# Kernel optimization log

Measured on AMD Instinct MI355X. Metric: run time of the kernel, lower is better.

The kernel has to match this reference:

```python
import jax, jax.numpy as jnp
import numpy as np

NUM_HEADS = 4
INITIAL_VALUE = 1.0
HEADS_RANGE = 3.0


def rotate_every_two(x):
    x1 = x[..., ::2]
    x2 = x[..., 1::2]
    return jnp.stack([-x2, x1], axis=-1).reshape(x.shape)


def theta_shift(x, sin, cos):
    return x * cos + rotate_every_two(x) * sin


def rel_pos_2d(h, w, key_dim):
    # angle: repeat each frequency twice -> length key_dim
    base = 1.0 / 10000.0 ** jnp.linspace(0.0, 1.0, key_dim // 2)
    angle = jnp.repeat(base, 2)
    decay = jnp.log(1.0 - 2.0 ** (-(INITIAL_VALUE + HEADS_RANGE * jnp.arange(NUM_HEADS, dtype=jnp.float32) / NUM_HEADS)))
    idx = jnp.arange(h * w, dtype=jnp.float32)
    sin = jnp.sin(idx[:, None] * angle[None, :]).reshape(h, w, key_dim)
    cos = jnp.cos(idx[:, None] * angle[None, :]).reshape(h, w, key_dim)
    def decay_1d(l):
        i = jnp.arange(l, dtype=jnp.float32)
        return jnp.abs(i[:, None] - i[None, :])[None, :, :] * decay[:, None, None]  # (n, l, l)
    return sin, cos, decay_1d(h), decay_1d(w)


def setup_inputs() -> dict:
    key = jax.random.key(0)
    b, C, H, W = 16, 256, 64, 64
    ks = jax.random.split(key, 12)
    gain = 2.0 ** (-2.5)
    xav = (2.0 / (C + C)) ** 0.5
    return {
        "x": jax.random.normal(ks[0], (b, C, H, W), jnp.float32),
        "Wq": jax.random.normal(ks[1], (C, C), jnp.float32) * gain * xav,
        "bq": jnp.zeros((C,), jnp.float32),
        "Wk": jax.random.normal(ks[2], (C, C), jnp.float32) * gain * xav,
        "bk": jnp.zeros((C,), jnp.float32),
        "Wv": jax.random.normal(ks[3], (C, C), jnp.float32) * gain * xav,
        "bv": jnp.zeros((C,), jnp.float32),
        "dw_kernel": jax.random.normal(ks[4], (5, 5, 1, C), jnp.float32) * 0.05,
        "dw_bias": jnp.zeros((C,), jnp.float32),
        "Wo": jax.random.normal(ks[5], (C, C), jnp.float32) * xav,
        "bo": jnp.zeros((C,), jnp.float32),
    }


def reference(x, Wq, bq, Wk, bk, Wv, bv, dw_kernel, dw_bias, Wo, bo):
    x = jnp.transpose(x, (0, 2, 3, 1))  # (b, h, w, c)
    b, h, w, c = x.shape
    n = NUM_HEADS
    d = c // n  # key_dim == head_dim (value_factor=1)
    scaling = d ** (-0.5)

    sin, cos, mask_h, mask_w = rel_pos_2d(h, w, d)

    q = x @ Wq + bq
    k = (x @ Wk + bk) * scaling
    v = x @ Wv + bv  # (b, h, w, c)

    # depthwise 5x5 conv (lepe) on v, NHWC
    lepe = jax.lax.conv_general_dilated(
        v, dw_kernel, window_strides=(1, 1), padding=((2, 2), (2, 2)),
        dimension_numbers=("NHWC", "HWIO", "NHWC"), feature_group_count=c,
    ) + dw_bias

    q = q.reshape(b, h, w, n, d).transpose(0, 3, 1, 2, 4)  # (b, n, h, w, d)
    k = k.reshape(b, h, w, n, d).transpose(0, 3, 1, 2, 4)
    qr = theta_shift(q, sin, cos)  # sin/cos (h,w,d) broadcast
    kr = theta_shift(k, sin, cos)

    # width-axis attention: rows independent
    qr_w = qr.transpose(0, 2, 1, 3, 4)  # (b, h, n, w, d)
    kr_w = kr.transpose(0, 2, 1, 3, 4)
    v5 = v.reshape(b, h, w, n, d).transpose(0, 1, 3, 2, 4)  # (b, h, n, w, d)
    qk_w = jnp.einsum("bhnqd,bhnkd->bhnqk", qr_w, kr_w) + mask_w  # (b,h,n,w,w)
    v5 = jnp.einsum("bhnqk,bhnkd->bhnqd", jax.nn.softmax(qk_w, axis=-1), v5)

    # height-axis attention: columns independent
    qr_h = qr.transpose(0, 3, 1, 2, 4)  # (b, w, n, h, d)
    kr_h = kr.transpose(0, 3, 1, 2, 4)
    v6 = v5.transpose(0, 3, 2, 1, 4)  # (b, w, n, h, d)
    qk_h = jnp.einsum("bwnqd,bwnkd->bwnqk", qr_h, kr_h) + mask_h  # (b,w,n,h,h)
    out = jnp.einsum("bwnqk,bwnkd->bwnqd", jax.nn.softmax(qk_h, axis=-1), v6)

    out = out.transpose(0, 3, 1, 2, 4).reshape(b, h, w, c)  # (b,h,w,n*d)
    out = (out + lepe) @ Wo + bo
    return jnp.transpose(out, (0, 3, 1, 2))  # (b, c, h, w)
```

## Files before the change

### kernel.cpp

```cpp
#include <hip/hip_runtime.h>
#include <hip/hip_bf16.h>

typedef unsigned short u16;
typedef unsigned int   u32;
typedef __attribute__((ext_vector_type(8))) short bf16x8;
typedef __attribute__((ext_vector_type(4))) float f32x4;

__device__ __forceinline__ float bf2f(u16 u) {
    union { u32 i; float f; } x; x.i = ((u32)u) << 16; return x.f;
}
__device__ __forceinline__ u16 f2bf(float f) {
    union { float f; u32 i; } x; x.f = f;
    u32 i = x.i;
    u32 r = (i + 0x7fffu + ((i >> 16) & 1u)) >> 16;
    return (u16)r;
}

__device__ __forceinline__ void gload16(const void* g, void* l) {
    __builtin_amdgcn_global_load_lds(
        (const __attribute__((address_space(1))) void*)g,
        (__attribute__((address_space(3))) void*)l, 16, 0, 0);
}

__global__ void k_tables(float2* __restrict__ csT) {
    int id = blockIdx.x * 256 + threadIdx.x;
    int t = id >> 5, i = id & 31;
    double ang = pow(10000.0, -(double)i / 31.0);
    double a = (double)t * ang;
    csT[id] = make_float2((float)cos(a), (float)sin(a));
}

__global__ __launch_bounds__(256) void k_prep_w(
    const float* __restrict__ Wq, const float* __restrict__ Wk,
    const float* __restrict__ Wv, const float* __restrict__ Wo,
    u16* __restrict__ WTq, u16* __restrict__ WTk,
    u16* __restrict__ WTv, u16* __restrict__ WoT)
{
    __shared__ float T[32][33];
    int z = blockIdx.z;
    const float* W = (z == 0) ? Wq : (z == 1) ? Wk : (z == 2) ? Wv : Wo;
    u16* WT        = (z == 0) ? WTq : (z == 1) ? WTk : (z == 2) ? WTv : WoT;
    int n0 = blockIdx.x * 32, k0 = blockIdx.y * 32;
    int tx = threadIdx.x & 31, ty = threadIdx.x >> 5;
#pragma unroll
    for (int i = 0; i < 4; i++)
        T[ty * 4 + i][tx] = W[(k0 + ty * 4 + i) * 256 + n0 + tx];
    __syncthreads();
#pragma unroll
    for (int i = 0; i < 4; i++)
        WT[(n0 + ty * 4 + i) * 256 + k0 + tx] = f2bf(T[tx][ty * 4 + i]);
}

__global__ __launch_bounds__(512, 1) void k_qkv_fused(
    const float* __restrict__ x, const u16* __restrict__ WTall,
    const float* __restrict__ bq, const float* __restrict__ bk,
    const float* __restrict__ bv,
    const float2* __restrict__ csT,
    u16* __restrict__ qr, u16* __restrict__ kr, u16* __restrict__ vO,
    u16* __restrict__ v5)
{
    __shared__ alignas(16) char smem[163840];
    u16* Alds = (u16*)smem;
    u16* BldsA[2] = { (u16*)(smem + 65536),
                      (u16*)(smem + 98304) };
    float2* SL = (float2*)(smem + 131072);

    const int tid = threadIdx.x;
    const int t0 = blockIdx.x * 128;
    const int lane = tid & 63, w = tid >> 6;

    const int srcChunk = (lane & 7) ^ (lane >> 3);
    const int rowInGrp = lane >> 3;

    {
        float* Bf = (float*)(smem + 65536);
        const int b0 = t0 >> 12, sb0 = t0 & 4095;
        const float* xb = x + ((size_t)b0 * 256) * 4096 + sb0;
#pragma unroll
        for (int ch = 0; ch < 2; ++ch) {
#pragma unroll
            for (int p = 0; p < 8; ++p) {
                int it = p * 512 + tid;
                int c = it >> 5, s4 = (it & 31) * 4;
                float4 v4 = *(const float4*)(xb + (size_t)(ch * 128 + c) * 4096 + s4);
                *(float4*)(Bf + c * 128 + s4) = v4;
            }
            __syncthreads();
#pragma unroll
            for (int p = 0; p < 4; ++p) {
                int it = p * 512 + tid;
                int tok = it & 127, ck = it >> 7;
                u16 tmp[8];
#pragma unroll
                for (int j = 0; j < 8; ++j)
                    tmp[j] = f2bf(Bf[(ck * 8 + j) * 128 + tok]);
                int gc = ch * 16 + ck;
                int gcs = (gc & 24) | ((gc & 7) ^ (tok & 7));
                *(bf16x8*)(Alds + tok * 256 + gcs * 8) = *(bf16x8*)tmp;
            }
            __syncthreads();
        }
    }

#pragma unroll
    for (int q = 0; q < 4; ++q) {
        int rl = (w * 4 + q) * 8 + rowInGrp;
        gload16(WTall + (size_t)rl * 256 + srcChunk * 8,
                BldsA[0] + (size_t)(w * 4 + q) * 512);
    }

    {
        const int sb = t0 & 4095;
#pragma unroll
        for (int p = 0; p < 8; ++p) {
            int idx = p * 512 + tid;
            SL[idx] = csT[(size_t)sb * 32 + idx];
        }
    }
    __syncthreads();

    const int wr = w >> 2, wc = w & 3;
    const int l15 = lane & 15, l4 = lane >> 4, l7 = lane & 7;

    f32x4 acc[4][4];

#pragma unroll
    for (int mat = 0; mat < 3; ++mat) {
#pragma unroll
        for (int mi = 0; mi < 4; ++mi)
#pragma unroll
            for (int ni = 0; ni < 4; ++ni) acc[mi][ni] = (f32x4)0.f;

#pragma unroll
        for (int ks = 0; ks < 4; ++ks) {
            const int s = mat * 4 + ks;
            u16* Bl = BldsA[s & 1];
            if (s < 11) {
                const int s2 = s + 1;
                const int mat2 = s2 >> 2, ks2 = s2 & 3;
#pragma unroll
                for (int q = 0; q < 4; ++q) {
                    int rl = (w * 4 + q) * 8 + rowInGrp;
                    gload16(WTall + (size_t)mat2 * 65536 + (size_t)rl * 256 +
                                ks2 * 64 + srcChunk * 8,
                            BldsA[s2 & 1] + (size_t)(w * 4 + q) * 512);
                }
            }
#pragma unroll
            for (int kk = 0; kk < 2; ++kk) {
                bf16x8 af[4], bfr[4];
#pragma unroll
                for (int mi = 0; mi < 4; ++mi) {
                    int r = wr * 64 + mi * 16 + l15;
                    af[mi] = *(const bf16x8*)(Alds + r * 256 + (ks * 8 + ((kk * 4 + l4) ^ l7)) * 8);
                }
#pragma unroll
                for (int ni = 0; ni < 4; ++ni) {
                    int r = wc * 64 + ni * 16 + l15;
                    bfr[ni] = *(const bf16x8*)(Bl + r * 64 + ((kk * 4 + l4) ^ l7) * 8);
                }
#pragma unroll
                for (int mi = 0; mi < 4; ++mi)
#pragma unroll
                    for (int ni = 0; ni < 4; ++ni)
                        acc[mi][ni] = __builtin_amdgcn_mfma_f32_16x16x32_bf16(
                            af[mi], bfr[ni], acc[mi][ni], 0, 0, 0);
            }
            __syncthreads();
        }

        const float* bias = (mat == 0) ? bq : (mat == 1) ? bk : bv;
        u16* out          = (mat == 0) ? qr : (mat == 1) ? kr : vO;
        const float kscale = (mat == 1) ? 0.125f : 1.0f;
        float bcol[4]; int ip[4];
#pragma unroll
        for (int ni = 0; ni < 4; ++ni) {
            bcol[ni] = bias[wc * 64 + ni * 16 + l15];
            ip[ni] = (ni * 16 + l15) >> 1;
        }
#pragma unroll
        for (int mi = 0; mi < 4; ++mi) {
#pragma unroll
            for (int rg = 0; rg < 4; ++rg) {
                const int sl = wr * 64 + mi * 16 + l4 * 4 + rg;
                size_t trow = (size_t)(t0 + sl) * 256;
#pragma unroll
                for (int ni = 0; ni < 4; ++ni) {
                    float val = (acc[mi][ni][rg] + bcol[ni]) * kscale;
                    float prt = __shfl_xor(val, 1);
                    float res, res2;
                    if (mat != 2) {
                        float2 cs = SL[sl * 32 + ip[ni]];
                        res  = fmaf(val, cs.x, -prt * cs.y);
                        res2 = fmaf(prt, cs.x,  val * cs.y);
                    } else {
                        res = val; res2 = prt;
                    }
                    if (!(lane & 1)) {
                        u32 pk;
                        asm("v_cvt_pk_bf16_f32 %0, %1, %2" : "=v"(pk) : "v"(res), "v"(res2));
                        int o = wc * 64 + ni * 16 + l15;
                        *(u32*)(out + trow + o) = pk;
                    }
                }
            }
        }
    }

    __syncthreads();
    u16* VTl = (u16*)smem + w * 4608;
    u16* PLl = (u16*)(smem + 73728) + w * 4608;

    {
        float bcv[4];
#pragma unroll
        for (int ni = 0; ni < 4; ++ni) bcv[ni] = bv[wc * 64 + ni * 16 + l15];
#pragma unroll
        for (int mi = 0; mi < 4; ++mi)
#pragma unroll
            for (int ni = 0; ni < 4; ++ni) {
                int d = ni * 16 + l15;
                int gs = (mi * 2 + (l4 >> 1)) ^ (d >> 3);
                float e0 = acc[mi][ni][0] + bcv[ni], e1 = acc[mi][ni][1] + bcv[ni];
                float e2 = acc[mi][ni][2] + bcv[ni], e3 = acc[mi][ni][3] + bcv[ni];
                u32 p0, p1;
                asm("v_cvt_pk_bf16_f32 %0, %1, %2" : "=v"(p0) : "v"(e0), "v"(e1));
                asm("v_cvt_pk_bf16_f32 %0, %1, %2" : "=v"(p1) : "v"(e2), "v"(e3));
                uint2 pp; pp.x = p0; pp.y = p1;
                *(uint2*)(VTl + d * 72 + gs * 8 + (l4 & 1) * 4) = pp;
            }
    }

    asm volatile("s_waitcnt vmcnt(0)" ::: "memory");
    const size_t qkb = (size_t)(t0 + wr * 64) * 256 + wc * 64;
    bf16x8 ka[4][2], qb[4][2];
#pragma unroll
    for (int t = 0; t < 4; ++t)
#pragma unroll
        for (int ks = 0; ks < 2; ++ks) {
            ka[t][ks] = *(const bf16x8*)(kr + qkb + (size_t)(t * 16 + l15) * 256 + ks * 32 + l4 * 8);
            qb[t][ks] = *(const bf16x8*)(qr + qkb + (size_t)(t * 16 + l15) * 256 + ks * 32 + l4 * 8);
        }

    f32x4 sacc[4][4];
#pragma unroll
    for (int kt = 0; kt < 4; ++kt)
#pragma unroll
        for (int qt = 0; qt < 4; ++qt) sacc[kt][qt] = (f32x4)0.f;
#pragma unroll
    for (int ks = 0; ks < 2; ++ks)
#pragma unroll
        for (int kt = 0; kt < 4; ++kt)
#pragma unroll
            for (int qt = 0; qt < 4; ++qt)
                sacc[kt][qt] = __builtin_amdgcn_mfma_f32_16x16x32_bf16(
                    ka[kt][ks], qb[qt][ks], sacc[kt][qt], 0, 0, 0);

    const float decay = logf(1.0f - exp2f(-(1.0f + 0.75f * (float)wc)));
#pragma unroll
    for (int qt = 0; qt < 4; ++qt) {
        const int qq = qt * 16 + l15;
        float lsum = 0.f;
#pragma unroll
        for (int kt = 0; kt < 4; ++kt) {
            const int kb = kt * 16 + l4 * 4;
#pragma unroll
            for (int rr = 0; rr < 4; ++rr) {
                float s = sacc[kt][qt][rr] + fabsf((float)(qq - kb - rr)) * decay;
                s = __expf(s);
                sacc[kt][qt][rr] = s;
                lsum += s;
            }
        }
        lsum += __shfl_xor(lsum, 16);
        lsum += __shfl_xor(lsum, 32);
        const float rinv = 1.0f / lsum;
#pragma unroll
        for (int kt = 0; kt < 4; ++kt) {
            float e0 = sacc[kt][qt][0] * rinv, e1 = sacc[kt][qt][1] * rinv;
            float e2 = sacc[kt][qt][2] * rinv, e3 = sacc[kt][qt][3] * rinv;
            u32 p0, p1;
            asm("v_cvt_pk_bf16_f32 %0, %1, %2" : "=v"(p0) : "v"(e0), "v"(e1));
            asm("v_cvt_pk_bf16_f32 %0, %1, %2" : "=v"(p1) : "v"(e2), "v"(e3));
            uint2 pp; pp.x = p0; pp.y = p1;
            *(uint2*)(PLl + (qt * 16 + l15) * 72 + kt * 16 + l4 * 4) = pp;
        }
    }

    __builtin_amdgcn_s_waitcnt(0xC07F);
    bf16x8 pa[4][2], vb[4][2];
#pragma unroll
    for (int qt = 0; qt < 4; ++qt)
#pragma unroll
        for (int ks = 0; ks < 2; ++ks)
            pa[qt][ks] = *(const bf16x8*)(PLl + (qt * 16 + l15) * 72 + ks * 32 + l4 * 8);
#pragma unroll
    for (int dt = 0; dt < 4; ++dt)
#pragma unroll
        for (int ks = 0; ks < 2; ++ks) {
            int d = dt * 16 + l15;
            int g = (ks * 4 + l4) ^ (d >> 3);
            vb[dt][ks] = *(const bf16x8*)(VTl + d * 72 + g * 8);
        }

    f32x4 oacc[4][4];
#pragma unroll
    for (int qt = 0; qt < 4; ++qt)
#pragma unroll
        for (int dt = 0; dt < 4; ++dt) oacc[qt][dt] = (f32x4)0.f;
#pragma unroll
    for (int ks = 0; ks < 2; ++ks)
#pragma unroll
        for (int qt = 0; qt < 4; ++qt)
#pragma unroll
            for (int dt = 0; dt < 4; ++dt)
                oacc[qt][dt] = __builtin_amdgcn_mfma_f32_16x16x32_bf16(
                    pa[qt][ks], vb[dt][ks], oacc[qt][dt], 0, 0, 0);

#pragma unroll
    for (int qt = 0; qt < 4; ++qt)
#pragma unroll
        for (int dt = 0; dt < 4; ++dt)
#pragma unroll
            for (int rr = 0; rr < 4; ++rr)
                PLl[(qt * 16 + l4 * 4 + rr) * 72 + dt * 16 + l15] = f2bf(oacc[qt][dt][rr]);
    __builtin_amdgcn_s_waitcnt(0xC07F);

    const int b0 = t0 >> 12;
    const int line = ((t0 & 4095) >> 6) + wr;
    size_t orow = ((size_t)((b0 * 64 + lane) * 4 + wc)) * 4096 + line * 64;
#pragma unroll
    for (int c = 0; c < 8; ++c)
        *(bf16x8*)(v5 + orow + c * 8) = *(const bf16x8*)(PLl + lane * 72 + c * 8);
}

__global__ __launch_bounds__(256) void k_lepe(
    const u16* __restrict__ v, const float* __restrict__ dwk,
    const float* __restrict__ dwb, u16* __restrict__ lepe)
{
    __shared__ u16 VhU[12 * 12 * 64];
    __shared__ float Kl[25][64];
    const int b = blockIdx.z, cg = blockIdx.y * 64;
    const int ty0 = (blockIdx.x >> 3) * 8, tx0 = (blockIdx.x & 7) * 8;
    const int tid = threadIdx.x;

    for (int idx = tid; idx < 1600; idx += 256) {
        int tap = idx >> 6, c = idx & 63;
        Kl[tap][c] = dwk[tap * 256 + cg + c];
    }
#pragma unroll
    for (int p = 0; p < 9; ++p) {
        int idx = p * 256 + tid;
        int ch = idx & 15, pos = idx >> 4;
        int py = pos / 12, px = pos - py * 12;
        int gy = ty0 + py - 2, gx = tx0 + px - 2;
        ushort4 val = make_ushort4(0, 0, 0, 0);
        if (gy >= 0 && gy < 64 && gx >= 0 && gx < 64)
            val = *(const ushort4*)(v + (size_t)(b * 4096 + gy * 64 + gx) * 256 + cg + ch * 4);
        *(ushort4*)(VhU + pos * 64 + ch * 4) = val;
    }
    __syncthreads();

    const int c = tid & 63, pg = tid >> 6;
    float kreg[25];
#pragma unroll
    for (int t = 0; t < 25; t++) kreg[t] = Kl[t][c];
    const float bias = dwb[cg + c];

    float acc[2][8];
#pragma unroll
    for (int t = 0; t < 2; ++t)
#pragma unroll
        for (int ox = 0; ox < 8; ++ox) acc[t][ox] = bias;

#pragma unroll
    for (int rr = 0; rr < 6; ++rr) {
        const int r = pg * 2 + rr;
        float rv[12];
#pragma unroll
        for (int px = 0; px < 12; ++px)
            rv[px] = bf2f(VhU[(r * 12 + px) * 64 + c]);
        if (rr <= 4) {
            const int dy = rr;
#pragma unroll
            for (int ox = 0; ox < 8; ++ox)
#pragma unroll
                for (int dx = 0; dx < 5; ++dx)
                    acc[0][ox] = fmaf(rv[ox + dx], kreg[dy * 5 + dx], acc[0][ox]);
        }
        if (rr >= 1) {
            const int dy = rr - 1;
#pragma unroll
            for (int ox = 0; ox < 8; ++ox)
#pragma unroll
                for (int dx = 0; dx < 5; ++dx)
                    acc[1][ox] = fmaf(rv[ox + dx], kreg[dy * 5 + dx], acc[1][ox]);
        }
    }

#pragma unroll
    for (int t = 0; t < 2; ++t) {
        const int oy = pg * 2 + t;
#pragma unroll
        for (int ox = 0; ox < 8; ++ox)
            lepe[(size_t)(b * 4096 + (ty0 + oy) * 64 + tx0 + ox) * 256 + cg + c] =
                f2bf(acc[t][ox]);
    }
}

__global__ __launch_bounds__(256) void k_attn_h(
    const u16* __restrict__ qr, const u16* __restrict__ kr,
    const u16* __restrict__ vsrc, const u16* __restrict__ lepeP,
    u16* __restrict__ outb)
{
    __shared__ u16 VT[4][64 * 72];
    __shared__ u16 PL[4][64 * 72];

    const int tid = threadIdx.x;
    const int w = tid >> 6, lane = tid & 63;
    const int l15 = lane & 15, l4 = lane >> 4;
    const int wid = blockIdx.x * 4 + w;
    const int b = wid >> 8, xy = (wid >> 2) & 63, n = wid & 3;

    const size_t qkbase = ((size_t)(b * 4096 + xy)) * 256 + n * 64;
    const int qkstride = 64 * 256;
    const size_t vbase = ((size_t)((b * 64 + xy) * 4 + n)) * 4096;
    const int vstride = 64;

    u16* VTl = &VT[w][0];
    u16* PLl = &PL[w][0];

    bf16x8 vld[8];
    const int vrow = lane >> 3, vchunk = lane & 7;
#pragma unroll
    for (int it = 0; it < 8; ++it)
        vld[it] = *(const bf16x8*)(vsrc + vbase + (size_t)(it * 8 + vrow) * vstride + vchunk * 8);

    bf16x8 ka[4][2], qb[4][2];
#pragma unroll
    for (int t = 0; t < 4; ++t)
#pragma unroll
        for (int ks = 0; ks < 2; ++ks) {
            ka[t][ks] = *(const bf16x8*)(kr + qkbase + (size_t)(t * 16 + l15) * qkstride + ks * 32 + l4 * 8);
            qb[t][ks] = *(const bf16x8*)(qr + qkbase + (size_t)(t * 16 + l15) * qkstride + ks * 32 + l4 * 8);
        }

    f32x4 sacc[4][4];
#pragma unroll
    for (int kt = 0; kt < 4; ++kt)
#pragma unroll
        for (int qt = 0; qt < 4; ++qt) sacc[kt][qt] = (f32x4)0.f;
#pragma unroll
    for (int ks = 0; ks < 2; ++ks)
#pragma unroll
        for (int kt = 0; kt < 4; ++kt)
#pragma unroll
            for (int qt = 0; qt < 4; ++qt)
                sacc[kt][qt] = __builtin_amdgcn_mfma_f32_16x16x32_bf16(
                    ka[kt][ks], qb[qt][ks], sacc[kt][qt], 0, 0, 0);

#pragma unroll
    for (int it = 0; it < 8; ++it) {
        int gp = ((it ^ vchunk) << 3) + vrow;
#pragma unroll
        for (int j = 0; j < 8; ++j) {
            int d = vchunk * 8 + j;
            VTl[d * 72 + gp] = (u16)vld[it][j];
        }
    }

    const float decay = logf(1.0f - exp2f(-(1.0f + 0.75f * (float)n)));
#pragma unroll
    for (int qt = 0; qt < 4; ++qt) {
        const int qq = qt * 16 + l15;
        float lsum = 0.f;
#pragma unroll
        for (int kt = 0; kt < 4; ++kt) {
            const int kb = kt * 16 + l4 * 4;
#pragma unroll
            for (int rr = 0; rr < 4; ++rr) {
                float s = sacc[kt][qt][rr] + fabsf((float)(qq - kb - rr)) * decay;
                s = __expf(s);
                sacc[kt][qt][rr] = s;
                lsum += s;
            }
        }
        lsum += __shfl_xor(lsum, 16);
        lsum += __shfl_xor(lsum, 32);
        const float rinv = 1.0f / lsum;
#pragma unroll
        for (int kt = 0; kt < 4; ++kt) {
            float e0 = sacc[kt][qt][0] * rinv, e1 = sacc[kt][qt][1] * rinv;
            float e2 = sacc[kt][qt][2] * rinv, e3 = sacc[kt][qt][3] * rinv;
            u32 p0, p1;
            asm("v_cvt_pk_bf16_f32 %0, %1, %2" : "=v"(p0) : "v"(e0), "v"(e1));
            asm("v_cvt_pk_bf16_f32 %0, %1, %2" : "=v"(p1) : "v"(e2), "v"(e3));
            uint2 pp; pp.x = p0; pp.y = p1;
            *(uint2*)(PLl + (qt * 16 + l15) * 72 + kt * 16 + l4 * 4) = pp;
        }
    }

    __builtin_amdgcn_s_waitcnt(0xC07F);
    bf16x8 pa[4][2], vb[4][2];
#pragma unroll
    for (int qt = 0; qt < 4; ++qt)
#pragma unroll
        for (int ks = 0; ks < 2; ++ks)
            pa[qt][ks] = *(const bf16x8*)(PLl + (qt * 16 + l15) * 72 + ks * 32 + l4 * 8);
#pragma unroll
    for (int dt = 0; dt < 4; ++dt)
#pragma unroll
        for (int ks = 0; ks < 2; ++ks) {
            int d = dt * 16 + l15;
            int g = (ks * 4 + l4) ^ (d >> 3);
            vb[dt][ks] = *(const bf16x8*)(VTl + d * 72 + g * 8);
        }

    f32x4 oacc[4][4];
#pragma unroll
    for (int qt = 0; qt < 4; ++qt)
#pragma unroll
        for (int dt = 0; dt < 4; ++dt) oacc[qt][dt] = (f32x4)0.f;
#pragma unroll
    for (int ks = 0; ks < 2; ++ks)
#pragma unroll
        for (int qt = 0; qt < 4; ++qt)
#pragma unroll
            for (int dt = 0; dt < 4; ++dt)
                oacc[qt][dt] = __builtin_amdgcn_mfma_f32_16x16x32_bf16(
                    pa[qt][ks], vb[dt][ks], oacc[qt][dt], 0, 0, 0);

#pragma unroll
    for (int qt = 0; qt < 4; ++qt)
#pragma unroll
        for (int dt = 0; dt < 4; ++dt)
#pragma unroll
            for (int rr = 0; rr < 4; ++rr)
                PLl[(qt * 16 + l4 * 4 + rr) * 72 + dt * 16 + l15] = f2bf(oacc[qt][dt][rr]);
    __builtin_amdgcn_s_waitcnt(0xC07F);

    size_t orow = ((size_t)(b * 4096 + lane * 64 + xy)) * 256 + n * 64;
#pragma unroll
    for (int c = 0; c < 8; ++c) {
        bf16x8 o8 = *(const bf16x8*)(PLl + lane * 72 + c * 8);
        bf16x8 lp = *(const bf16x8*)(lepeP + orow + c * 8);
        u16 hv[8];
#pragma unroll
        for (int j = 0; j < 8; ++j)
            hv[j] = f2bf(bf2f((u16)o8[j]) + bf2f((u16)lp[j]));
        *(bf16x8*)(outb + orow + c * 8) = *(bf16x8*)hv;
    }
}

__global__ __launch_bounds__(512, 1) void k_proj_fused(
    const u16* __restrict__ WoT, const u16* __restrict__ attnL,
    const float* __restrict__ bo, float* __restrict__ y)
{
    __shared__ alignas(16) u16 Alds[128 * 256];
    __shared__ alignas(16) u16 Blds[2][256 * 64];

    const int tid = threadIdx.x;
    const int bid = blockIdx.x;
    const int xcd = bid & 7, slot = bid >> 3;
    const int tt = xcd * 32 + (slot >> 1);
    const int oh = slot & 1;
    const int t0 = tt * 256;
    const int o0 = oh * 128;

    const int lane = tid & 63, w = tid >> 6;
    const int srcChunk = (lane & 7) ^ (lane >> 3);
    const int rowInGrp = lane >> 3;
    const int ar = tid >> 5, ac = tid & 31;

#pragma unroll
    for (int q = 0; q < 4; ++q) {
        int rl = (w * 4 + q) * 8 + rowInGrp;
        gload16(attnL + (size_t)(t0 + rl) * 256 + srcChunk * 8,
                &Blds[0][0] + (size_t)(w * 4 + q) * 512);
    }
    {
        bf16x8 areg[8];
#pragma unroll
        for (int p = 0; p < 8; ++p)
            areg[p] = *(const bf16x8*)(WoT + (size_t)(o0 + p * 16 + ar) * 256 + ac * 8);
#pragma unroll
        for (int p = 0; p < 8; ++p) {
            int r = p * 16 + ar;
            *(bf16x8*)(Alds + r * 256 + (ac ^ (r & 7)) * 8) = areg[p];
        }
    }
    __syncthreads();

    const int wr = w >> 2, wc = w & 3;
    const int l15 = lane & 15, l4 = lane >> 4, l7 = lane & 7;

    f32x4 acc[4][4];
#pragma unroll
    for (int mi = 0; mi < 4; ++mi)
#pragma unroll
        for (int ni = 0; ni < 4; ++ni) acc[mi][ni] = (f32x4)0.f;

#pragma unroll
    for (int ks = 0; ks < 4; ++ks) {
        u16* Bl = &Blds[ks & 1][0];
        if (ks < 3) {
#pragma unroll
            for (int q = 0; q < 4; ++q) {
                int rl = (w * 4 + q) * 8 + rowInGrp;
                gload16(attnL + (size_t)(t0 + rl) * 256 + (ks + 1) * 64 + srcChunk * 8,
                        &Blds[(ks + 1) & 1][0] + (size_t)(w * 4 + q) * 512);
            }
        }
#pragma unroll
        for (int kk = 0; kk < 2; ++kk) {
            bf16x8 af[4], bfr[4];
#pragma unroll
            for (int mi = 0; mi < 4; ++mi) {
                int r = wr * 64 + mi * 16 + l15;
                af[mi] = *(const bf16x8*)(Alds + r * 256 + (ks * 8 + ((kk * 4 + l4) ^ l7)) * 8);
            }
#pragma unroll
            for (int ni = 0; ni < 4; ++ni) {
                int r = wc * 64 + ni * 16 + l15;
                bfr[ni] = *(const bf16x8*)(Bl + r * 64 + ((kk * 4 + l4) ^ l7) * 8);
            }
#pragma unroll
            for (int mi = 0; mi < 4; ++mi)
#pragma unroll
                for (int ni = 0; ni < 4; ++ni)
                    acc[mi][ni] = __builtin_amdgcn_mfma_f32_16x16x32_bf16(
                        af[mi], bfr[ni], acc[mi][ni], 0, 0, 0);
        }
        __syncthreads();
    }

    const int b = t0 >> 12, sb = t0 & 4095;
#pragma unroll
    for (int mi = 0; mi < 4; ++mi) {
#pragma unroll
        for (int rg = 0; rg < 4; ++rg) {
            int o = o0 + wr * 64 + mi * 16 + l4 * 4 + rg;
            float bb = bo[o];
            float* yrow = y + ((size_t)(b * 256 + o)) * 4096 + sb + wc * 64;
#pragma unroll
            for (int ni = 0; ni < 4; ++ni)
                yrow[ni * 16 + l15] = acc[mi][ni][rg] + bb;
        }
    }
}

extern "C" void kernel_launch(void* const* d_in, const int* in_sizes, int n_in,
                              void* d_out, int out_size, void* d_ws, size_t ws_size,
                              hipStream_t stream)
{
    const float* x   = (const float*)d_in[0];
    const float* Wq  = (const float*)d_in[1];
    const float* bq  = (const float*)d_in[2];
    const float* Wk  = (const float*)d_in[3];
    const float* bk  = (const float*)d_in[4];
    const float* Wv  = (const float*)d_in[5];
    const float* bv  = (const float*)d_in[6];
    const float* dwk = (const float*)d_in[7];
    const float* dwb = (const float*)d_in[8];
    const float* Wo  = (const float*)d_in[9];
    const float* bo  = (const float*)d_in[10];
    float* y = (float*)d_out;

    char* ws = (char*)d_ws;
    const size_t MB = 1024 * 1024;
    float2* csT = (float2*)(ws);
    u16* WTq = (u16*)(ws + 1 * MB);
    u16* WTk = WTq + 65536;
    u16* WTv = WTk + 65536;
    u16* WoT = WTv + 65536;
    u16* qr   = (u16*)(ws + 2 * MB);
    u16* kr   = (u16*)(ws + 2 * MB + 32 * MB);
    u16* v    = (u16*)(ws + 2 * MB + 64 * MB);
    u16* lepe = (u16*)(ws + 2 * MB + 96 * MB);
    u16* v5   = (u16*)(ws + 2 * MB + 128 * MB);
    u16* attn = v;

    k_tables<<<dim3(512), dim3(256), 0, stream>>>(csT);
    k_prep_w<<<dim3(8, 8, 4), dim3(256), 0, stream>>>(Wq, Wk, Wv, Wo, WTq, WTk, WTv, WoT);
    k_qkv_fused<<<dim3(512), dim3(512), 0, stream>>>(
        x, WTq, bq, bk, bv, csT, qr, kr, v, v5);
    k_lepe<<<dim3(64, 4, 16), dim3(256), 0, stream>>>(v, dwk, dwb, lepe);
    k_attn_h<<<dim3(1024), dim3(256), 0, stream>>>(qr, kr, v5, lepe, attn);
    k_proj_fused<<<dim3(512), dim3(512), 0, stream>>>(WoT, attn, bo, y);
}
```

Baseline: 187.9 us.

## Merge table and weight-prep kernels, read cos/sin from global, add MFMA priority

Folds the cos/sin table kernel and the weight transpose kernel into one launch split by block index, removing one kernel launch. In the QKV kernel the 32 KB LDS staging of the cos/sin table is dropped and values are read directly from global memory in the epilogue, cutting LDS use and a staging pass. In the attention kernel the MFMA loops are wrapped with s_setprio to raise wave priority during matrix work. The direct global reads may add latency in the epilogue.

```diff
diff --git a/kernel.cpp b/kernel.cpp
--- a/kernel.cpp
+++ b/kernel.cpp
@@ -22,25 +22,28 @@
         (__attribute__((address_space(3))) void*)l, 16, 0, 0);
 }
 
-__global__ void k_tables(float2* __restrict__ csT) {
-    int id = blockIdx.x * 256 + threadIdx.x;
-    int t = id >> 5, i = id & 31;
-    double ang = pow(10000.0, -(double)i / 31.0);
-    double a = (double)t * ang;
-    csT[id] = make_float2((float)cos(a), (float)sin(a));
-}
-
-__global__ __launch_bounds__(256) void k_prep_w(
+__global__ __launch_bounds__(256) void k_init(
+    float2* __restrict__ csT,
     const float* __restrict__ Wq, const float* __restrict__ Wk,
     const float* __restrict__ Wv, const float* __restrict__ Wo,
     u16* __restrict__ WTq, u16* __restrict__ WTk,
     u16* __restrict__ WTv, u16* __restrict__ WoT)
 {
+    const int bid = blockIdx.x;
+    if (bid < 512) {
+        int id = bid * 256 + threadIdx.x;
+        int t = id >> 5, i = id & 31;
+        double ang = pow(10000.0, -(double)i / 31.0);
+        double a = (double)t * ang;
+        csT[id] = make_float2((float)cos(a), (float)sin(a));
+        return;
+    }
     __shared__ float T[32][33];
-    int z = blockIdx.z;
+    const int fid = bid - 512;
+    const int bx = fid & 7, by = (fid >> 3) & 7, z = fid >> 6;
     const float* W = (z == 0) ? Wq : (z == 1) ? Wk : (z == 2) ? Wv : Wo;
     u16* WT        = (z == 0) ? WTq : (z == 1) ? WTk : (z == 2) ? WTv : WoT;
-    int n0 = blockIdx.x * 32, k0 = blockIdx.y * 32;
+    int n0 = bx * 32, k0 = by * 32;
     int tx = threadIdx.x & 31, ty = threadIdx.x >> 5;
 #pragma unroll
     for (int i = 0; i < 4; i++)
@@ -59,11 +62,10 @@
     u16* __restrict__ qr, u16* __restrict__ kr, u16* __restrict__ vO,
     u16* __restrict__ v5)
 {
-    __shared__ alignas(16) char smem[163840];
+    __shared__ alignas(16) char smem[147456];
     u16* Alds = (u16*)smem;
     u16* BldsA[2] = { (u16*)(smem + 65536),
                       (u16*)(smem + 98304) };
-    float2* SL = (float2*)(smem + 131072);
 
     const int tid = threadIdx.x;
     const int t0 = blockIdx.x * 128;
@@ -108,19 +110,11 @@
         gload16(WTall + (size_t)rl * 256 + srcChunk * 8,
                 BldsA[0] + (size_t)(w * 4 + q) * 512);
     }
-
-    {
-        const int sb = t0 & 4095;
-#pragma unroll
-        for (int p = 0; p < 8; ++p) {
-            int idx = p * 512 + tid;
-            SL[idx] = csT[(size_t)sb * 32 + idx];
-        }
-    }
     __syncthreads();
 
     const int wr = w >> 2, wc = w & 3;
     const int l15 = lane & 15, l4 = lane >> 4, l7 = lane & 7;
+    const int sb = t0 & 4095;
 
     f32x4 acc[4][4];
 
@@ -190,7 +184,7 @@
                     float prt = __shfl_xor(val, 1);
                     float res, res2;
                     if (mat != 2) {
-                        float2 cs = SL[sl * 32 + ip[ni]];
+                        float2 cs = csT[(size_t)(sb + sl) * 32 + ip[ni]];
                         res  = fmaf(val, cs.x, -prt * cs.y);
                         res2 = fmaf(prt, cs.x,  val * cs.y);
                     } else {
@@ -450,6 +444,7 @@
     for (int kt = 0; kt < 4; ++kt)
 #pragma unroll
         for (int qt = 0; qt < 4; ++qt) sacc[kt][qt] = (f32x4)0.f;
+    __builtin_amdgcn_s_setprio(1);
 #pragma unroll
     for (int ks = 0; ks < 2; ++ks)
 #pragma unroll
@@ -458,6 +453,7 @@
             for (int qt = 0; qt < 4; ++qt)
                 sacc[kt][qt] = __builtin_amdgcn_mfma_f32_16x16x32_bf16(
                     ka[kt][ks], qb[qt][ks], sacc[kt][qt], 0, 0, 0);
+    __builtin_amdgcn_s_setprio(0);
 
 #pragma unroll
     for (int it = 0; it < 8; ++it) {
@@ -521,6 +517,7 @@
     for (int qt = 0; qt < 4; ++qt)
 #pragma unroll
         for (int dt = 0; dt < 4; ++dt) oacc[qt][dt] = (f32x4)0.f;
+    __builtin_amdgcn_s_setprio(1);
 #pragma unroll
     for (int ks = 0; ks < 2; ++ks)
 #pragma unroll
@@ -529,6 +526,7 @@
             for (int dt = 0; dt < 4; ++dt)
                 oacc[qt][dt] = __builtin_amdgcn_mfma_f32_16x16x32_bf16(
                     pa[qt][ks], vb[dt][ks], oacc[qt][dt], 0, 0, 0);
+    __builtin_amdgcn_s_setprio(0);
 
 #pragma unroll
     for (int qt = 0; qt < 4; ++qt)
@@ -680,8 +678,8 @@
     u16* v5   = (u16*)(ws + 2 * MB + 128 * MB);
     u16* attn = v;
 
-    k_tables<<<dim3(512), dim3(256), 0, stream>>>(csT);
-    k_prep_w<<<dim3(8, 8, 4), dim3(256), 0, stream>>>(Wq, Wk, Wv, Wo, WTq, WTk, WTv, WoT);
+    k_init<<<dim3(768), dim3(256), 0, stream>>>(
+        csT, Wq, Wk, Wv, Wo, WTq, WTk, WTv, WoT);
     k_qkv_fused<<<dim3(512), dim3(512), 0, stream>>>(
         x, WTq, bq, bk, bv, csT, qr, kr, v, v5);
     k_lepe<<<dim3(64, 4, 16), dim3(256), 0, stream>>>(v, dwk, dwb, lepe);
```

Measured after the change: 218.5 us. 1.16x slower.
